# Optimization experiments

Measured on AMD Instinct MI355X. Metric: run time of the kernel, lower is better.

The kernel has to match this reference:

```python
import jax, jax.numpy as jnp
import numpy as np
from functools import partial

LEAK = 1.0 / 3.0   # scn default leakiness 0.333
EPS = 1e-4         # scn BatchNormalization default eps


def linkey(c, S):
    return (c[..., 0] * S + c[..., 1]) * S + c[..., 2]


def sub_offsets(K):
    r = K // 2
    g = np.stack(np.meshgrid(*([np.arange(-r, r + 1)] * 3), indexing='ij'), -1).reshape(-1, 3)
    return jnp.asarray(g, jnp.int32)


def down_offsets(s):
    g = np.stack(np.meshgrid(*([np.arange(s)] * 3), indexing='ij'), -1).reshape(-1, 3)
    return jnp.asarray(g, jnp.int32)


@partial(jax.checkpoint, static_argnums=(4, 5))
def sparse_conv(out_coords, in_coords, in_feats, W, S_in, stride, offsets):
    """Rulebook gather-GEMM-scatter via sorted-key binary search.
    out_coords [M,3], in_coords [N,3] sorted by linearized key, in_feats [N,Cin],
    W [K3,Cin,Cout]. Submanifold: stride=1, centered offsets, out_coords==in_coords.
    Strided scn.Convolution: offsets 0..stride-1, out sites = unique(in//stride)."""
    in_keys = linkey(in_coords, S_in)  # sorted [N]
    Nin = in_keys.shape[0]

    def body(acc, kw):
        off, Wk = kw
        child = out_coords * stride + off                       # [M,3]
        valid = jnp.all((child >= 0) & (child < S_in), axis=-1)
        nkey = linkey(child, S_in)
        idx = jnp.searchsorted(in_keys, nkey)
        idxc = jnp.clip(idx, 0, Nin - 1)
        found = valid & (in_keys[idxc] == nkey)
        g = jnp.where(found[:, None], in_feats[idxc], 0.0)      # gather, zero for inactive
        return acc + g @ Wk, None

    acc0 = jnp.zeros((out_coords.shape[0], W.shape[-1]), in_feats.dtype)
    acc, _ = jax.lax.scan(body, acc0, (offsets, W))
    return acc


def bn_lrelu(x, g, b):
    m = x.mean(0)
    v = x.var(0)
    y = (x - m) * (g / jnp.sqrt(v + EPS)) + b
    return jnp.where(y > 0, y, LEAK * y)


def lrelu(x):
    return jnp.where(x > 0, x, LEAK * x)


def forward_core(floats, c0, c1, c2, c3, c4):
    (feats0, W_init, Wd1, gd1, bd1, W11a, g11, b11, W11b,
     W12a, g12, b12, W12b, Wd2, gd2, bd2,
     W21a, g21, b21, W21b, W22a, g22, b22, W22b,
     Wd3, gd3, bd3, Wd4, gd4, bd4, W2, b2, W3, b3) = floats
    o3 = sub_offsets(3)
    x = sparse_conv(c0, c0, feats0, W_init, 512, 1, sub_offsets(7))                 # [N0,64] @512
    x = bn_lrelu(sparse_conv(c1, c0, x, Wd1, 512, 2, down_offsets(2)), gd1, bd1)    # [N1,64] @256
    res = x
    h = bn_lrelu(sparse_conv(c1, c1, x, W11a, 256, 1, o3), g11, b11)
    x = lrelu(sparse_conv(c1, c1, h, W11b, 256, 1, o3) + res)
    res = x
    h = bn_lrelu(sparse_conv(c1, c1, x, W12a, 256, 1, o3), g12, b12)
    x = lrelu(sparse_conv(c1, c1, h, W12b, 256, 1, o3) + res)
    x = bn_lrelu(sparse_conv(c2, c1, x, Wd2, 256, 2, down_offsets(2)), gd2, bd2)    # [N2,128] @128
    res = x
    h = bn_lrelu(sparse_conv(c2, c2, x, W21a, 128, 1, o3), g21, b21)
    x = lrelu(sparse_conv(c2, c2, h, W21b, 128, 1, o3) + res)
    res = x
    h = bn_lrelu(sparse_conv(c2, c2, x, W22a, 128, 1, o3), g22, b22)
    x = lrelu(sparse_conv(c2, c2, h, W22b, 128, 1, o3) + res)
    x = bn_lrelu(sparse_conv(c3, c2, x, Wd3, 128, 4, down_offsets(4)), gd3, bd3)    # [N3,64] @32
    x = bn_lrelu(sparse_conv(c4, c3, x, Wd4, 32, 4, down_offsets(4)), gd4, bd4)     # [N4,2]  @8
    # SparseToDense -> dense [2,8,8,8], then torch .view(-1, 2*8*8*8) (channel-major)
    k4 = linkey(c4, 8)
    dense = jnp.zeros((8 * 8 * 8, 2), x.dtype).at[k4].set(x)    # [512,2]
    flat = dense.T.reshape(1, -1)                               # [1,1024]
    v = jax.nn.elu(flat @ W2 + b2)
    return jax.nn.sigmoid(v @ W3 + b3)                          # [1,1]


def _decode(k, S):
    a = k // (S * S)
    r = k % (S * S)
    return np.stack([a, r // S, r % S], -1).astype(np.int32)


def setup_inputs() -> dict:
    rng = np.random.default_rng(0)
    N0 = 50000
    k0 = np.unique(rng.integers(0, 512 ** 3, size=N0 + 20000))[:N0]
    c0 = _decode(k0, 512)
    c1 = _decode(np.unique((c0[:, 0].astype(np.int64) // 2 * 256 + c0[:, 1] // 2) * 256 + c0[:, 2] // 2), 256)
    c2 = _decode(np.unique((c1[:, 0].astype(np.int64) // 2 * 128 + c1[:, 1] // 2) * 128 + c1[:, 2] // 2), 128)
    c3 = _decode(np.unique((c2[:, 0].astype(np.int64) // 4 * 32 + c2[:, 1] // 4) * 32 + c2[:, 2] // 4), 32)
    c4 = _decode(np.unique((c3[:, 0].astype(np.int64) // 4 * 8 + c3[:, 1] // 4) * 8 + c3[:, 2] // 4), 8)
    key = jax.random.key(0)
    ks = jax.random.split(key, 20)

    def w(i, shape, fan):
        return jax.random.normal(ks[i], shape, jnp.float32) / np.float32(np.sqrt(fan))

    return dict(
        feats0=jax.random.normal(ks[0], (N0, 1), jnp.float32),
        W_init=w(1, (343, 1, 64), 343.0),
        Wd1=w(2, (8, 64, 64), 8 * 64), gd1=jnp.ones(64), bd1=jnp.zeros(64),
        W11a=w(3, (27, 64, 64), 27 * 64), g11=jnp.ones(64), b11=jnp.zeros(64),
        W11b=w(4, (27, 64, 64), 27 * 64),
        W12a=w(5, (27, 64, 64), 27 * 64), g12=jnp.ones(64), b12=jnp.zeros(64),
        W12b=w(6, (27, 64, 64), 27 * 64),
        Wd2=w(7, (8, 64, 128), 8 * 64), gd2=jnp.ones(128), bd2=jnp.zeros(128),
        W21a=w(8, (27, 128, 128), 27 * 128), g21=jnp.ones(128), b21=jnp.zeros(128),
        W21b=w(9, (27, 128, 128), 27 * 128),
        W22a=w(10, (27, 128, 128), 27 * 128), g22=jnp.ones(128), b22=jnp.zeros(128),
        W22b=w(11, (27, 128, 128), 27 * 128),
        Wd3=w(12, (64, 128, 64), 64 * 128), gd3=jnp.ones(64), bd3=jnp.zeros(64),
        Wd4=w(13, (64, 64, 2), 64 * 64), gd4=jnp.ones(2), bd4=jnp.zeros(2),
        W2=w(14, (1024, 2), 1024.0), b2=jnp.zeros(2),
        W3=w(15, (2, 1), 2.0), b3=jnp.zeros(1),
        coords0=jnp.asarray(c0), coords1=jnp.asarray(c1), coords2=jnp.asarray(c2),
        coords3=jnp.asarray(c3), coords4=jnp.asarray(c4),
    )


def reference(feats0, W_init, Wd1, gd1, bd1, W11a, g11, b11, W11b, W12a, g12, b12, W12b,
              Wd2, gd2, bd2, W21a, g21, b21, W21b, W22a, g22, b22, W22b,
              Wd3, gd3, bd3, Wd4, gd4, bd4, W2, b2, W3, b3,
              coords0, coords1, coords2, coords3, coords4):
    floats = (feats0, W_init, Wd1, gd1, bd1, W11a, g11, b11, W11b, W12a, g12, b12, W12b,
              Wd2, gd2, bd2, W21a, g21, b21, W21b, W22a, g22, b22, W22b,
              Wd3, gd3, bd3, Wd4, gd4, bd4, W2, b2, W3, b3)
    return forward_core(floats, coords0, coords1, coords2, coords3, coords4)
```

## Files before the change

kernel.cpp:

```cpp
#include <hip/hip_runtime.h>

#define LEAKF (1.0f/3.0f)
#define BN_EPS 1e-4f

__device__ __forceinline__ unsigned hmix(int key) {
    unsigned h = (unsigned)key * 2654435761u;
    h ^= h >> 15;
    return h;
}

__device__ __forceinline__ int hlookup(const int* __restrict__ hk,
                                       const int* __restrict__ hv,
                                       int mask, int key) {
    unsigned h = hmix(key) & (unsigned)mask;
    while (true) {
        int k = hk[h];
        if (k == key) return hv[h];
        if (k == -1) return -1;
        h = (h + 1) & (unsigned)mask;
    }
}

__device__ __forceinline__ float bnl(float v, float s, float h) {
    v = v * s + h;
    return v > 0.f ? v : v * LEAKF;
}

__global__ __launch_bounds__(256) void build_hash_bm_all(
    int B0, int B1, int B2,
    int N0, const int* __restrict__ c0, int* __restrict__ hk0, int* __restrict__ hv0,
    int m0, unsigned* __restrict__ bm0,
    int N1, const int* __restrict__ c1, int* __restrict__ hk1, int* __restrict__ hv1,
    int m1, unsigned* __restrict__ bm1,
    int N2, const int* __restrict__ c2, int* __restrict__ hk2, int* __restrict__ hv2,
    int m2, unsigned* __restrict__ bm2,
    int N3, const int* __restrict__ c3, int* __restrict__ hk3, int* __restrict__ hv3,
    int m3) {
    const int* coords; int* hk; int* hv; unsigned* bm; int mask, S, N, i;
    int b = blockIdx.x;
    if (b < B0)           { coords = c0; hk = hk0; hv = hv0; bm = bm0; mask = m0; S = 512; N = N0; i = b * 256 + threadIdx.x; }
    else if (b < B0 + B1) { coords = c1; hk = hk1; hv = hv1; bm = bm1; mask = m1; S = 256; N = N1; i = (b - B0) * 256 + threadIdx.x; }
    else if (b < B0 + B1 + B2) { coords = c2; hk = hk2; hv = hv2; bm = bm2; mask = m2; S = 128; N = N2; i = (b - B0 - B1) * 256 + threadIdx.x; }
    else                  { coords = c3; hk = hk3; hv = hv3; bm = nullptr; mask = m3; S = 32; N = N3; i = (b - B0 - B1 - B2) * 256 + threadIdx.x; }
    if (i >= N) return;
    int key = (coords[3 * i] * S + coords[3 * i + 1]) * S + coords[3 * i + 2];
    if (bm) atomicOr(&bm[key >> 5], 1u << (key & 31));
    unsigned h = hmix(key) & (unsigned)mask;
    while (true) {
        int old = atomicCAS(&hk[h], -1, key);
        if (old == -1 || old == key) { hv[h] = i; break; }
        h = (h + 1) & (unsigned)mask;
    }
}

__global__ __launch_bounds__(256) void rb_sub_bm(
    int B1,
    int N1, const int* __restrict__ c1, const unsigned* __restrict__ bm1,
    const int* __restrict__ hk1, const int* __restrict__ hv1, int m1,
    int2* __restrict__ rb1, int* __restrict__ cnt1, int cap1,
    int N2, const int* __restrict__ c2, const unsigned* __restrict__ bm2,
    const int* __restrict__ hk2, const int* __restrict__ hv2, int m2,
    int2* __restrict__ rb2, int* __restrict__ cnt2, int cap2) {
    __shared__ int lcnt[27];
    __shared__ int lbase[27];
    int tid = threadIdx.x;
    if (tid < 27) lcnt[tid] = 0;
    __syncthreads();
    const int* coords; const unsigned* bm; const int* hk; const int* hv;
    int mask, S, N, t; int2* pairs; int* counts; int cap;
    if (blockIdx.x < B1) {
        coords = c1; bm = bm1; hk = hk1; hv = hv1; mask = m1; S = 256; N = N1;
        pairs = rb1; counts = cnt1; cap = cap1; t = blockIdx.x * 256 + tid;
    } else {
        coords = c2; bm = bm2; hk = hk2; hv = hv2; mask = m2; S = 128; N = N2;
        pairs = rb2; counts = cnt2; cap = cap2; t = (blockIdx.x - B1) * 256 + tid;
    }
    unsigned bits = 0;
    int m = 0, kmin = 0, z = 0, dx = 0, dy = 0;
    int rk[3], ix[3];
    if (t < N * 9) {
        m = t / 9;
        int od = t - m * 9;
        dx = od / 3 - 1;
        dy = od - (od / 3) * 3 - 1;
        int x = coords[3 * m] + dx;
        int y = coords[3 * m + 1] + dy;
        z = coords[3 * m + 2];
        if ((unsigned)x < (unsigned)S && (unsigned)y < (unsigned)S) {
            int zmin = z - 1 < 0 ? 0 : z - 1;
            int zmax = z + 1 > S - 1 ? S - 1 : z + 1;
            kmin = (x * S + y) * S + zmin;
            int wi = kmin >> 5, sh = kmin & 31, nb = zmax - zmin + 1;
            unsigned long long w =
                ((unsigned long long)bm[wi + 1] << 32) | (unsigned long long)bm[wi];
            bits = (unsigned)((w >> sh) & ((1u << nb) - 1u));
            if (dx == 0 && dy == 0) bits &= ~(1u << (z - zmin));
            unsigned tmp = bits;
            int nf = 0;
            while (tmp) {
                int bb = __ffs(tmp) - 1;
                tmp &= tmp - 1;
                ix[nf] = hlookup(hk, hv, mask, kmin + bb);
                int dz = (kmin & (S - 1)) + bb - z;
                int k = (dx + 1) * 9 + (dy + 1) * 3 + (dz + 1);
                rk[nf] = atomicAdd(&lcnt[k], 1);
                nf++;
            }
        }
    }
    __syncthreads();
    if (tid < 27 && lcnt[tid] > 0) lbase[tid] = atomicAdd(&counts[tid], lcnt[tid]);
    __syncthreads();
    {
        unsigned tmp = bits;
        int j = 0;
        while (tmp) {
            int bb = __ffs(tmp) - 1;
            tmp &= tmp - 1;
            int dz = (kmin & (S - 1)) + bb - z;
            int k = (dx + 1) * 9 + (dy + 1) * 3 + (dz + 1);
            int p = lbase[k] + rk[j];
            if (p < cap) pairs[(size_t)k * cap + p] = make_int2(m, ix[j]);
            j++;
        }
    }
}

__global__ __launch_bounds__(256) void rb_down_all(
    int B1, int B2,
    int N0, const int* __restrict__ c0, const int* __restrict__ hk1,
    const int* __restrict__ hv1, int m1, int2* __restrict__ rbD1,
    int* __restrict__ cntD1, int capD1,
    int N1, const int* __restrict__ c1, const int* __restrict__ hk2,
    const int* __restrict__ hv2, int m2, int2* __restrict__ rbD2,
    int* __restrict__ cntD2, int capD2,
    int N2, const int* __restrict__ c2, const int* __restrict__ hk3,
    const int* __restrict__ hv3, int m3, int2* __restrict__ rbD3,
    int* __restrict__ cntD3, int capD3) {
    __shared__ int lcnt[64];
    __shared__ int lbase[64];
    int tid = threadIdx.x;
    const int* cin; const int* hk; const int* hv;
    int mask, Sout, s, Nin, i; int2* pairs; int* counts; int cap;
    int b = blockIdx.x;
    if (b < B1) {
        cin = c0; hk = hk1; hv = hv1; mask = m1; Sout = 256; s = 2; Nin = N0;
        pairs = rbD1; counts = cntD1; cap = capD1; i = b * 256 + tid;
    } else if (b < B1 + B2) {
        cin = c1; hk = hk2; hv = hv2; mask = m2; Sout = 128; s = 2; Nin = N1;
        pairs = rbD2; counts = cntD2; cap = capD2; i = (b - B1) * 256 + tid;
    } else {
        cin = c2; hk = hk3; hv = hv3; mask = m3; Sout = 32; s = 4; Nin = N2;
        pairs = rbD3; counts = cntD3; cap = capD3; i = (b - B1 - B2) * 256 + tid;
    }
    int K3 = s * s * s;
    if (tid < K3) lcnt[tid] = 0;
    __syncthreads();
    int k = -1, m = -1, rank = 0;
    if (i < Nin) {
        int x = cin[3 * i], y = cin[3 * i + 1], z = cin[3 * i + 2];
        k = ((x % s) * s + (y % s)) * s + (z % s);
        int key = ((x / s) * Sout + (y / s)) * Sout + (z / s);
        m = hlookup(hk, hv, mask, key);
        rank = atomicAdd(&lcnt[k], 1);
    }
    __syncthreads();
    if (tid < K3 && lcnt[tid] > 0) lbase[tid] = atomicAdd(&counts[tid], lcnt[tid]);
    __syncthreads();
    if (i < Nin) {
        int p = lbase[k] + rank;
        if (p < cap) pairs[(size_t)k * cap + p] = make_int2(m, i);
    }
}

__global__ __launch_bounds__(256) void init_probe(
    int total, const int* __restrict__ c0, const unsigned* __restrict__ bm,
    const int* __restrict__ hk, const int* __restrict__ hv, int mask,
    int2* __restrict__ pairs, int* __restrict__ pcount, int cap) {
    __shared__ int lcnt, lbase;
    int tid = threadIdx.x;
    if (tid == 0) lcnt = 0;
    __syncthreads();
    int t = blockIdx.x * 256 + tid;
    unsigned bits = 0;
    int m = -1, kmin = 0, z = 0, dx = 0, dy = 0, rank = 0;
    if (t < total) {
        m = t / 49;
        int od = t - m * 49;
        dx = od / 7 - 3;
        dy = od - (od / 7) * 7 - 3;
        int x = c0[3 * m] + dx;
        int y = c0[3 * m + 1] + dy;
        z = c0[3 * m + 2];
        if ((unsigned)x < 512u && (unsigned)y < 512u) {
            int zmin = z - 3 < 0 ? 0 : z - 3;
            int zmax = z + 3 > 511 ? 511 : z + 3;
            kmin = (x * 512 + y) * 512 + zmin;
            int wi = kmin >> 5, sh = kmin & 31, nb = zmax - zmin + 1;
            unsigned long long w =
                ((unsigned long long)bm[wi + 1] << 32) | (unsigned long long)bm[wi];
            bits = (unsigned)((w >> sh) & ((1u << nb) - 1u));
            if (dx == 0 && dy == 0) bits &= ~(1u << (z - zmin));
            if (bits) rank = atomicAdd(&lcnt, __popc(bits));
        }
    }
    __syncthreads();
    if (tid == 0 && lcnt > 0) lbase = atomicAdd(pcount, lcnt);
    __syncthreads();
    while (bits) {
        int b = __ffs(bits) - 1;
        bits &= bits - 1;
        int nkey = kmin + b;
        int idx = hlookup(hk, hv, mask, nkey);
        int dz = (kmin & 511) + b - z;
        int k = (dx + 3) * 49 + (dy + 3) * 7 + (dz + 3);
        int p = lbase + rank++;
        if (p < cap) pairs[p] = make_int2(m, idx | (k << 17));
    }
}

__global__ __launch_bounds__(256) void init_center(
    int N0, const float* __restrict__ f0, const float* __restrict__ W,
    float* __restrict__ out) {
    int t = blockIdx.x * 256 + threadIdx.x;
    if (t >= N0 * 64) return;
    int m = t >> 6, co = t & 63;
    out[t] = f0[m] * W[171 * 64 + co];
}

__global__ __launch_bounds__(256) void init_apply(
    const int2* __restrict__ pairs, const int* __restrict__ pcount, int cap,
    const float* __restrict__ f0, const float* __restrict__ W,
    float* __restrict__ out) {
    int P = min(*pcount, cap);
    int t = blockIdx.x * 256 + threadIdx.x;
    if (t >= P * 64) return;
    int p = t >> 6, co = t & 63;
    int2 pr = pairs[p];
    int idx = pr.y & 0x1FFFF, k = pr.y >> 17;
    atomicAdd(&out[(size_t)pr.x * 64 + co], f0[idx] * W[k * 64 + co]);
}

template <int C, int TS, bool BNF>
__global__ __launch_bounds__(256) void center_gemm(
    int N, const float* __restrict__ inF, const float* __restrict__ Wc,
    float* __restrict__ out, const float* __restrict__ scp,
    const float* __restrict__ shp) {
    constexpr int C4 = C / 4;
    constexpr int SP = TS / 8;
    __shared__ float sW[C * 64];
    __shared__ float4 sRow[TS * C4];
    int tid = threadIdx.x;
    int t0 = blockIdx.x * TS;
    int co0 = blockIdx.y << 6;
    for (int e = tid; e < C * 16; e += 256) {
        int ci = e >> 4, c4 = e & 15;
        ((float4*)sW)[e] = *(const float4*)(Wc + (size_t)ci * C + co0 + c4 * 4);
    }
    for (int e = tid; e < TS * C4; e += 256) {
        int p = e / C4, c4 = e - p * C4;
        float4 v = make_float4(0.f, 0.f, 0.f, 0.f);
        if (t0 + p < N) {
            v = ((const float4*)inF)[(size_t)(t0 + p) * C4 + c4];
            if (BNF) {
                float4 s4 = ((const float4*)scp)[c4];
                float4 h4 = ((const float4*)shp)[c4];
                v.x = bnl(v.x, s4.x, h4.x);
                v.y = bnl(v.y, s4.y, h4.y);
                v.z = bnl(v.z, s4.z, h4.z);
                v.w = bnl(v.w, s4.w, h4.w);
            }
        }
        sRow[e] = v;
    }
    __syncthreads();
    int co = tid & 31, sg = tid >> 5;
    float accA[SP], accB[SP];
#pragma unroll
    for (int j = 0; j < SP; j++) { accA[j] = 0.f; accB[j] = 0.f; }
    for (int c4 = 0; c4 < C4; c4++) {
        float a0 = sW[(c4 * 4 + 0) * 64 + co];
        float a1 = sW[(c4 * 4 + 1) * 64 + co];
        float a2 = sW[(c4 * 4 + 2) * 64 + co];
        float a3 = sW[(c4 * 4 + 3) * 64 + co];
        float b0 = sW[(c4 * 4 + 0) * 64 + co + 32];
        float b1 = sW[(c4 * 4 + 1) * 64 + co + 32];
        float b2 = sW[(c4 * 4 + 2) * 64 + co + 32];
        float b3 = sW[(c4 * 4 + 3) * 64 + co + 32];
#pragma unroll
        for (int j = 0; j < SP; j++) {
            float4 r = sRow[(sg * SP + j) * C4 + c4];
            accA[j] += r.x * a0 + r.y * a1 + r.z * a2 + r.w * a3;
            accB[j] += r.x * b0 + r.y * b1 + r.z * b2 + r.w * b3;
        }
    }
#pragma unroll
    for (int j = 0; j < SP; j++) {
        int p = sg * SP + j;
        if (t0 + p < N) {
            out[(size_t)(t0 + p) * C + co0 + co] = accA[j];
            out[(size_t)(t0 + p) * C + co0 + co + 32] = accB[j];
        }
    }
}

template <int CIN, int P, bool BNF>
__global__ __launch_bounds__(256) void pair_gemm(
    const float* __restrict__ inF, const float* __restrict__ W, float* __restrict__ out,
    const int2* __restrict__ pairs, const int* __restrict__ counts,
    int cap, int chunksPerK, int COUT,
    const float* __restrict__ scp, const float* __restrict__ shp) {
    constexpr int C4 = CIN / 4;
    constexpr int SP = P / 8;
    __shared__ float sW[CIN * 64];
    __shared__ float4 sRow[P * C4];
    __shared__ int sM[P];
    __shared__ int sIdx[P];
    int k = blockIdx.x / chunksPerK;
    int chunk = blockIdx.x - k * chunksPerK;
    int cnt = min(counts[k], cap);
    int base = chunk * P;
    if (base >= cnt) return;
    int Pact = min(P, cnt - base);
    int tid = threadIdx.x;
    if (tid < P) {
        if (tid < Pact) {
            int2 pr = pairs[(size_t)k * cap + base + tid];
            sM[tid] = pr.x;
            sIdx[tid] = pr.y;
        } else {
            sM[tid] = -1;
            sIdx[tid] = 0;
        }
    }
    __syncthreads();
    int co0 = blockIdx.y << 6;
    const float* gW = W + (size_t)k * CIN * COUT + co0;
    for (int e = tid; e < CIN * 16; e += 256) {
        int ci = e >> 4, c4 = e & 15;
        ((float4*)sW)[e] = *(const float4*)(gW + (size_t)ci * COUT + c4 * 4);
    }
    for (int e = tid; e < P * C4; e += 256) {
        int p = e / C4, c4 = e - p * C4;
        float4 v = make_float4(0.f, 0.f, 0.f, 0.f);
        if (p < Pact) {
            v = ((const float4*)inF)[(size_t)sIdx[p] * C4 + c4];
            if (BNF) {
                float4 s4 = ((const float4*)scp)[c4];
                float4 h4 = ((const float4*)shp)[c4];
                v.x = bnl(v.x, s4.x, h4.x);
                v.y = bnl(v.y, s4.y, h4.y);
                v.z = bnl(v.z, s4.z, h4.z);
                v.w = bnl(v.w, s4.w, h4.w);
            }
        }
        sRow[e] = v;
    }
    __syncthreads();
    int co = tid & 31, sg = tid >> 5;
    float accA[SP], accB[SP];
#pragma unroll
    for (int j = 0; j < SP; j++) { accA[j] = 0.f; accB[j] = 0.f; }
    for (int c4 = 0; c4 < C4; c4++) {
        float a0 = sW[(c4 * 4 + 0) * 64 + co];
        float a1 = sW[(c4 * 4 + 1) * 64 + co];
        float a2 = sW[(c4 * 4 + 2) * 64 + co];
        float a3 = sW[(c4 * 4 + 3) * 64 + co];
        float b0 = sW[(c4 * 4 + 0) * 64 + co + 32];
        float b1 = sW[(c4 * 4 + 1) * 64 + co + 32];
        float b2 = sW[(c4 * 4 + 2) * 64 + co + 32];
        float b3 = sW[(c4 * 4 + 3) * 64 + co + 32];
#pragma unroll
        for (int j = 0; j < SP; j++) {
            float4 r = sRow[(sg * SP + j) * C4 + c4];
            accA[j] += r.x * a0 + r.y * a1 + r.z * a2 + r.w * a3;
            accB[j] += r.x * b0 + r.y * b1 + r.z * b2 + r.w * b3;
        }
    }
#pragma unroll
    for (int j = 0; j < SP; j++) {
        int p = sg * SP + j;
        if (p < Pact) {
            atomicAdd(&out[(size_t)sM[p] * COUT + co0 + co], accA[j]);
            atomicAdd(&out[(size_t)sM[p] * COUT + co0 + co + 32], accB[j]);
        }
    }
}

__global__ __launch_bounds__(64) void convd4_kernel(
    int M, const int* __restrict__ oc, const float* __restrict__ x3,
    const float* __restrict__ W, float* __restrict__ out4,
    const int* __restrict__ hk, const int* __restrict__ hv, int mask,
    const float* __restrict__ scp, const float* __restrict__ shp) {
    __shared__ int sIdx[64];
    __shared__ int sK[64];
    __shared__ int sCount;
    int m = blockIdx.x, tid = threadIdx.x;
    int cx = oc[3 * m], cy = oc[3 * m + 1], cz = oc[3 * m + 2];
    if (tid == 0) sCount = 0;
    __syncthreads();
    {
        int k = tid;
        int a = k >> 4, b = (k >> 2) & 3, c = k & 3;
        int x = cx * 4 + a, y = cy * 4 + b, z = cz * 4 + c;
        int key = (x * 32 + y) * 32 + z;
        int idx = hlookup(hk, hv, mask, key);
        if (idx >= 0) { int p = atomicAdd(&sCount, 1); sIdx[p] = idx; sK[p] = k; }
    }
    __syncthreads();
    int cnt = sCount;
    float s = scp[tid], h = shp[tid];
    float a0 = 0.f, a1 = 0.f;
    for (int j = 0; j < cnt; j++) {
        int idx = sIdx[j], k = sK[j];
        float f = bnl(x3[(size_t)idx * 64 + tid], s, h);
        const float* wk = W + ((size_t)k * 64 + tid) * 2;
        a0 += f * wk[0];
        a1 += f * wk[1];
    }
    for (int o = 32; o > 0; o >>= 1) {
        a0 += __shfl_down(a0, o);
        a1 += __shfl_down(a1, o);
    }
    if (tid == 0) { out4[2 * m] = a0; out4[2 * m + 1] = a1; }
}

__global__ __launch_bounds__(256) void bn_reduce_fin(
    const float4* __restrict__ X4, int total4, int B4, int C, int Cmask, float invN,
    const float* __restrict__ g, const float* __restrict__ b,
    float* __restrict__ sums, int* __restrict__ done,
    float* __restrict__ sc, float* __restrict__ sh) {
    __shared__ float sS[128];
    __shared__ float sQ[128];
    __shared__ int isLast;
    int tid = threadIdx.x;
    if (tid < C) { sS[tid] = 0.f; sQ[tid] = 0.f; }
    __syncthreads();
    int base4 = blockIdx.x * B4;
    int end4 = min(base4 + B4, total4);
    float s0 = 0.f, s1 = 0.f, s2 = 0.f, s3 = 0.f;
    float q0 = 0.f, q1 = 0.f, q2 = 0.f, q3 = 0.f;
    for (int e4 = base4 + tid; e4 < end4; e4 += 256) {
        float4 v = X4[e4];
        s0 += v.x; q0 += v.x * v.x;
        s1 += v.y; q1 += v.y * v.y;
        s2 += v.z; q2 += v.z * v.z;
        s3 += v.w; q3 += v.w * v.w;
    }
    int c0 = (4 * (base4 + tid)) & Cmask;
    atomicAdd(&sS[c0], s0);               atomicAdd(&sQ[c0], q0);
    atomicAdd(&sS[(c0 + 1) & Cmask], s1); atomicAdd(&sQ[(c0 + 1) & Cmask], q1);
    atomicAdd(&sS[(c0 + 2) & Cmask], s2); atomicAdd(&sQ[(c0 + 2) & Cmask], q2);
    atomicAdd(&sS[(c0 + 3) & Cmask], s3); atomicAdd(&sQ[(c0 + 3) & Cmask], q3);
    __syncthreads();
    if (tid < C) {
        atomicAdd(&sums[tid], sS[tid]);
        atomicAdd(&sums[128 + tid], sQ[tid]);
    }
    __syncthreads();
    if (tid == 0) {
        __threadfence();
        int t = atomicAdd(done, 1);
        isLast = (t == (int)gridDim.x - 1);
    }
    __syncthreads();
    if (isLast) {
        if (tid < C) {
            float v1 = atomicAdd(&sums[tid], 0.0f);
            float v2 = atomicAdd(&sums[128 + tid], 0.0f);
            float mean = v1 * invN;
            float var = v2 * invN - mean * mean;
            float s = g[tid] / sqrtf(var + BN_EPS);
            sc[tid] = s;
            sh[tid] = b[tid] - mean * s;
            sums[tid] = 0.f;
            sums[128 + tid] = 0.f;
        }
        if (tid == 0) *done = 0;
    }
}

__global__ __launch_bounds__(256) void add_lrelu(const float4* __restrict__ A,
                                                 const float4* __restrict__ R,
                                                 float4* __restrict__ Y, int total4) {
    int e = blockIdx.x * 256 + threadIdx.x;
    if (e >= total4) return;
    float4 a = A[e], r = R[e], v;
    v.x = a.x + r.x; v.y = a.y + r.y; v.z = a.z + r.z; v.w = a.w + r.w;
    v.x = v.x > 0.f ? v.x : v.x * LEAKF;
    v.y = v.y > 0.f ? v.y : v.y * LEAKF;
    v.z = v.z > 0.f ? v.z : v.z * LEAKF;
    v.w = v.w > 0.f ? v.w : v.w * LEAKF;
    Y[e] = v;
}

__global__ __launch_bounds__(256) void add_lrelu_bn(const float4* __restrict__ A,
                                                    const float4* __restrict__ X,
                                                    float4* __restrict__ Y, int total4,
                                                    int C4mask,
                                                    const float* __restrict__ scp,
                                                    const float* __restrict__ shp) {
    int e = blockIdx.x * 256 + threadIdx.x;
    if (e >= total4) return;
    int c4 = e & C4mask;
    float4 s4 = ((const float4*)scp)[c4];
    float4 h4 = ((const float4*)shp)[c4];
    float4 a = A[e], x = X[e], v;
    v.x = a.x + bnl(x.x, s4.x, h4.x);
    v.y = a.y + bnl(x.y, s4.y, h4.y);
    v.z = a.z + bnl(x.z, s4.z, h4.z);
    v.w = a.w + bnl(x.w, s4.w, h4.w);
    v.x = v.x > 0.f ? v.x : v.x * LEAKF;
    v.y = v.y > 0.f ? v.y : v.y * LEAKF;
    v.z = v.z > 0.f ? v.z : v.z * LEAKF;
    v.w = v.w > 0.f ? v.w : v.w * LEAKF;
    Y[e] = v;
}

__global__ __launch_bounds__(256) void bn_scatter(int M, const int* __restrict__ c4,
                                                  const float* __restrict__ x4,
                                                  const float* __restrict__ sc,
                                                  const float* __restrict__ sh,
                                                  float* __restrict__ dense) {
    int i = blockIdx.x * 256 + threadIdx.x;
    if (i >= 2 * M) return;
    int m = i >> 1, co = i & 1;
    float v = x4[i] * sc[co] + sh[co];
    v = v > 0.f ? v : v * LEAKF;
    int key = (c4[3 * m] * 8 + c4[3 * m + 1]) * 8 + c4[3 * m + 2];
    dense[key * 2 + co] = v;
}

__global__ __launch_bounds__(256) void head_kernel(const float* __restrict__ dense,
                                                   const float* __restrict__ W2,
                                                   const float* __restrict__ b2,
                                                   const float* __restrict__ W3,
                                                   const float* __restrict__ b3,
                                                   float* __restrict__ out) {
    __shared__ float r0[256];
    __shared__ float r1[256];
    int tid = threadIdx.x;
    float a0 = 0.f, a1 = 0.f;
    for (int j = tid; j < 1024; j += 256) {
        int co = j >> 9, k = j & 511;
        float f = dense[k * 2 + co];
        a0 += f * W2[2 * j];
        a1 += f * W2[2 * j + 1];
    }
    r0[tid] = a0;
    r1[tid] = a1;
    __syncthreads();
    for (int s = 128; s > 0; s >>= 1) {
        if (tid < s) { r0[tid] += r0[tid + s]; r1[tid] += r1[tid + s]; }
        __syncthreads();
    }
    if (tid == 0) {
        float v0 = r0[0] + b2[0];
        float v1 = r1[0] + b2[1];
        v0 = v0 > 0.f ? v0 : expm1f(v0);
        v1 = v1 > 0.f ? v1 : expm1f(v1);
        float z = v0 * W3[0] + v1 * W3[1] + b3[0];
        out[0] = 1.f / (1.f + expf(-z));
    }
}

extern "C" void kernel_launch(void* const* d_in, const int* in_sizes, int n_in,
                              void* d_out, int out_size, void* d_ws, size_t ws_size,
                              hipStream_t stream) {
    const float* F0    = (const float*)d_in[0];
    const float* Winit = (const float*)d_in[1];
    const float* Wd1   = (const float*)d_in[2];
    const float* gd1   = (const float*)d_in[3];
    const float* bd1   = (const float*)d_in[4];
    const float* W11a  = (const float*)d_in[5];
    const float* g11   = (const float*)d_in[6];
    const float* b11   = (const float*)d_in[7];
    const float* W11b  = (const float*)d_in[8];
    const float* W12a  = (const float*)d_in[9];
    const float* g12   = (const float*)d_in[10];
    const float* b12   = (const float*)d_in[11];
    const float* W12b  = (const float*)d_in[12];
    const float* Wd2   = (const float*)d_in[13];
    const float* gd2   = (const float*)d_in[14];
    const float* bd2   = (const float*)d_in[15];
    const float* W21a  = (const float*)d_in[16];
    const float* g21   = (const float*)d_in[17];
    const float* b21   = (const float*)d_in[18];
    const float* W21b  = (const float*)d_in[19];
    const float* W22a  = (const float*)d_in[20];
    const float* g22   = (const float*)d_in[21];
    const float* b22   = (const float*)d_in[22];
    const float* W22b  = (const float*)d_in[23];
    const float* Wd3   = (const float*)d_in[24];
    const float* gd3   = (const float*)d_in[25];
    const float* bd3   = (const float*)d_in[26];
    const float* Wd4   = (const float*)d_in[27];
    const float* gd4   = (const float*)d_in[28];
    const float* bd4   = (const float*)d_in[29];
    const float* W2    = (const float*)d_in[30];
    const float* b2    = (const float*)d_in[31];
    const float* W3    = (const float*)d_in[32];
    const float* b3    = (const float*)d_in[33];
    const int* c0 = (const int*)d_in[34];
    const int* c1 = (const int*)d_in[35];
    const int* c2 = (const int*)d_in[36];
    const int* c3 = (const int*)d_in[37];
    const int* c4 = (const int*)d_in[38];
    int N0 = in_sizes[34] / 3, N1 = in_sizes[35] / 3, N2 = in_sizes[36] / 3;
    int N3 = in_sizes[37] / 3, N4 = in_sizes[38] / 3;

    char* base = (char*)d_ws;
    size_t off = 0;
    auto alloc = [&](size_t bytes) -> void* {
        void* p = base + off;
        off = (off + bytes + 255) & ~(size_t)255;
        return p;
    };
    const int CAP0 = 262144, CAP = 131072, CAP3 = 65536;
    size_t hs_off = off;
    int* hk0 = (int*)alloc((size_t)CAP0 * 4);
    int* hv0 = (int*)alloc((size_t)CAP0 * 4);
    int* hk1 = (int*)alloc((size_t)CAP * 4);
    int* hv1 = (int*)alloc((size_t)CAP * 4);
    int* hk2 = (int*)alloc((size_t)CAP * 4);
    int* hv2 = (int*)alloc((size_t)CAP * 4);
    int* hk3 = (int*)alloc((size_t)CAP3 * 4);
    int* hv3 = (int*)alloc((size_t)CAP3 * 4);
    size_t he_off = off;
    size_t zs_off = off;
    float* sums = (float*)alloc(256 * 4);
    float* scb = (float*)alloc(8 * 128 * 4);
    float* shb = (float*)alloc(8 * 128 * 4);
    float* dense = (float*)alloc(1024 * 4);
    float* x4 = (float*)alloc(1032 * 4);
    int* counts = (int*)alloc(136 * 4);
    unsigned* bm1 = (unsigned*)alloc((size_t)(524288 + 2) * 4);
    unsigned* bm2 = (unsigned*)alloc((size_t)(65536 + 2) * 4);
    size_t ze_off = off;
    int* cntS1 = counts, *cntS2 = counts + 27, *cntD1 = counts + 54, *cntD2 = counts + 62,
       * cntD3 = counts + 70;
    int* done = counts + 134;
    int* pcount = counts + 135;
    const int CAP_S1 = 1024, CAP_S2 = 4096, CAP_D1 = 8192, CAP_D2 = 8192, CAP_D3 = 1024;
    const int CAPP = 16384;
    int2* pairs0 = (int2*)alloc((size_t)CAPP * 8);
    int2* rbS1 = (int2*)alloc((size_t)27 * CAP_S1 * 8);
    int2* rbS2 = (int2*)alloc((size_t)27 * CAP_S2 * 8);
    int2* rbD1 = (int2*)alloc((size_t)8 * CAP_D1 * 8);
    int2* rbD2 = (int2*)alloc((size_t)8 * CAP_D2 * 8);
    int2* rbD3 = (int2*)alloc((size_t)64 * CAP_D3 * 8);
    size_t relems = (size_t)N0 * 64;
    if ((size_t)N2 * 128 > relems) relems = (size_t)N2 * 128;
    float* R1 = (float*)alloc(relems * 4);
    float* R2 = (float*)alloc(relems * 4);
    float* R3 = (float*)alloc(relems * 4);
    unsigned* bm0 = (unsigned*)R1;

    hipMemsetAsync(base + hs_off, 0xFF, he_off - hs_off, stream);
    hipMemsetAsync(base + zs_off, 0x00, ze_off - zs_off, stream);
    hipMemsetAsync(bm0, 0x00, (size_t)(1 << 24) + 64, stream);

    int Bh0 = (N0 + 255) / 256, Bh1 = (N1 + 255) / 256, Bh2 = (N2 + 255) / 256,
        Bh3 = (N3 + 255) / 256;
    build_hash_bm_all<<<Bh0 + Bh1 + Bh2 + Bh3, 256, 0, stream>>>(
        Bh0, Bh1, Bh2,
        N0, c0, hk0, hv0, CAP0 - 1, bm0,
        N1, c1, hk1, hv1, CAP - 1, bm1,
        N2, c2, hk2, hv2, CAP - 1, bm2,
        N3, c3, hk3, hv3, CAP3 - 1);
    int Bs1 = (N1 * 9 + 255) / 256, Bs2 = (N2 * 9 + 255) / 256;
    rb_sub_bm<<<Bs1 + Bs2, 256, 0, stream>>>(
        Bs1,
        N1, c1, bm1, hk1, hv1, CAP - 1, rbS1, cntS1, CAP_S1,
        N2, c2, bm2, hk2, hv2, CAP - 1, rbS2, cntS2, CAP_S2);
    rb_down_all<<<Bh0 + Bh1 + Bh2, 256, 0, stream>>>(
        Bh0, Bh1,
        N0, c0, hk1, hv1, CAP - 1, rbD1, cntD1, CAP_D1,
        N1, c1, hk2, hv2, CAP - 1, rbD2, cntD2, CAP_D2,
        N2, c2, hk3, hv3, CAP3 - 1, rbD3, cntD3, CAP_D3);

    auto bnstats = [&](const float* X, int N, int C, const float* g, const float* b,
                       int slot) {
        int total4 = (N * C + 3) >> 2;
        int B4 = 32 * C;
        int grid = (total4 + B4 - 1) / B4;
        bn_reduce_fin<<<grid, 256, 0, stream>>>((const float4*)X, total4, B4, C, C - 1,
                                                1.0f / (float)N, g, b, sums, done,
                                                scb + slot * 128, shb + slot * 128);
    };
    auto sub64 = [&](const float* X, const float* W, float* Y, int slot) {
        if (slot >= 0) {
            center_gemm<64, 64, true><<<dim3((N1 + 63) / 64, 1), 256, 0, stream>>>(
                N1, X, W + 13 * 64 * 64, Y, scb + slot * 128, shb + slot * 128);
            pair_gemm<64, 64, true><<<dim3(27 * (CAP_S1 / 64), 1), 256, 0, stream>>>(
                X, W, Y, rbS1, cntS1, CAP_S1, CAP_S1 / 64, 64,
                scb + slot * 128, shb + slot * 128);
        } else {
            center_gemm<64, 64, false><<<dim3((N1 + 63) / 64, 1), 256, 0, stream>>>(
                N1, X, W + 13 * 64 * 64, Y, nullptr, nullptr);
            pair_gemm<64, 64, false><<<dim3(27 * (CAP_S1 / 64), 1), 256, 0, stream>>>(
                X, W, Y, rbS1, cntS1, CAP_S1, CAP_S1 / 64, 64, nullptr, nullptr);
        }
    };
    auto sub128 = [&](const float* X, const float* W, float* Y, int slot) {
        const int CH2 = (CAP_S2 + 47) / 48;
        if (slot >= 0) {
            center_gemm<128, 48, true><<<dim3((N2 + 47) / 48, 2), 256, 0, stream>>>(
                N2, X, W + 13 * 128 * 128, Y, scb + slot * 128, shb + slot * 128);
            pair_gemm<128, 48, true><<<dim3(27 * CH2, 2), 256, 0, stream>>>(
                X, W, Y, rbS2, cntS2, CAP_S2, CH2, 128, scb + slot * 128, shb + slot * 128);
        } else {
            center_gemm<128, 48, false><<<dim3((N2 + 47) / 48, 2), 256, 0, stream>>>(
                N2, X, W + 13 * 128 * 128, Y, nullptr, nullptr);
            pair_gemm<128, 48, false><<<dim3(27 * CH2, 2), 256, 0, stream>>>(
                X, W, Y, rbS2, cntS2, CAP_S2, CH2, 128, nullptr, nullptr);
        }
    };

    int totProbe = N0 * 49;
    init_probe<<<(totProbe + 255) / 256, 256, 0, stream>>>(totProbe, c0, bm0,
                                                           hk0, hv0, CAP0 - 1,
                                                           pairs0, pcount, CAPP);
    init_center<<<(N0 * 64 + 255) / 256, 256, 0, stream>>>(N0, F0, Winit, R3);
    init_apply<<<(CAPP * 64) / 256, 256, 0, stream>>>(pairs0, pcount, CAPP, F0, Winit, R3);

    hipMemsetAsync(R1, 0, (size_t)N1 * 64 * 4, stream);
    pair_gemm<64, 64, false><<<dim3(8 * (CAP_D1 / 64), 1), 256, 0, stream>>>(
        R3, Wd1, R1, rbD1, cntD1, CAP_D1, CAP_D1 / 64, 64, nullptr, nullptr);
    bnstats(R1, N1, 64, gd1, bd1, 0);

    sub64(R1, W11a, R2, 0);
    bnstats(R2, N1, 64, g11, b11, 1);
    sub64(R2, W11b, R3, 1);
    add_lrelu_bn<<<(N1 * 16 + 255) / 256, 256, 0, stream>>>(
        (const float4*)R3, (const float4*)R1, (float4*)R2, N1 * 16, 15, scb, shb);
    sub64(R2, W12a, R3, -1);
    bnstats(R3, N1, 64, g12, b12, 2);
    sub64(R3, W12b, R1, 2);
    add_lrelu<<<(N1 * 16 + 255) / 256, 256, 0, stream>>>(
        (const float4*)R1, (const float4*)R2, (float4*)R2, N1 * 16);

    hipMemsetAsync(R1, 0, (size_t)N2 * 128 * 4, stream);
    pair_gemm<64, 64, false><<<dim3(8 * (CAP_D2 / 64), 2), 256, 0, stream>>>(
        R2, Wd2, R1, rbD2, cntD2, CAP_D2, CAP_D2 / 64, 128, nullptr, nullptr);
    bnstats(R1, N2, 128, gd2, bd2, 3);

    sub128(R1, W21a, R2, 3);
    bnstats(R2, N2, 128, g21, b21, 4);
    sub128(R2, W21b, R3, 4);
    add_lrelu_bn<<<(N2 * 32 + 255) / 256, 256, 0, stream>>>(
        (const float4*)R3, (const float4*)R1, (float4*)R2, N2 * 32, 31,
        scb + 3 * 128, shb + 3 * 128);
    sub128(R2, W22a, R3, -1);
    bnstats(R3, N2, 128, g22, b22, 5);
    sub128(R3, W22b, R1, 5);
    add_lrelu<<<(N2 * 32 + 255) / 256, 256, 0, stream>>>(
        (const float4*)R1, (const float4*)R2, (float4*)R3, N2 * 32);

    hipMemsetAsync(R1, 0, (size_t)N3 * 64 * 4, stream);
    {
        const int CH3 = (CAP_D3 + 47) / 48;
        pair_gemm<128, 48, false><<<dim3(64 * CH3, 1), 256, 0, stream>>>(
            R3, Wd3, R1, rbD3, cntD3, CAP_D3, CH3, 64, nullptr, nullptr);
    }
    bnstats(R1, N3, 64, gd3, bd3, 6);

    convd4_kernel<<<N4, 64, 0, stream>>>(N4, c4, R1, Wd4, x4, hk3, hv3, CAP3 - 1,
                                         scb + 6 * 128, shb + 6 * 128);
    bnstats(x4, N4, 2, gd4, bd4, 7);
    bn_scatter<<<(2 * N4 + 255) / 256, 256, 0, stream>>>(N4, c4, x4, scb + 7 * 128,
                                                         shb + 7 * 128, dense);

    head_kernel<<<1, 256, 0, stream>>>(dense, W2, b2, W3, b3, (float*)d_out);
}
```

Baseline: 1.123 ms.

## Fuse residual add+LReLU into downsample gathers, enlarge GEMM tiles, swizzle probe blocks

Removes the two standalone add_lrelu kernels by computing residual add plus leaky ReLU on the fly while gathering rows in the following strided pair_gemm (new MODE=2). Buffer roles are reshuffled to match. Pair and center GEMM tile sizes grow (64→128 rows for C=64, 48→80 for C=128), and init_probe blocks are remapped in interleaved chunks of eight. Fusing saves a full read-write pass but recomputes the add for each of the 8 or 64 offsets. The larger tiles use more shared memory and registers per block.

```diff
diff --git a/kernel.cpp b/kernel.cpp
--- a/kernel.cpp
+++ b/kernel.cpp
@@ -174,14 +174,16 @@
 }
 
 __global__ __launch_bounds__(256) void init_probe(
-    int total, const int* __restrict__ c0, const unsigned* __restrict__ bm,
+    int total, int chunk, const int* __restrict__ c0, const unsigned* __restrict__ bm,
     const int* __restrict__ hk, const int* __restrict__ hv, int mask,
     int2* __restrict__ pairs, int* __restrict__ pcount, int cap) {
     __shared__ int lcnt, lbase;
     int tid = threadIdx.x;
     if (tid == 0) lcnt = 0;
     __syncthreads();
-    int t = blockIdx.x * 256 + tid;
+    int b = blockIdx.x;
+    int nb = (b & 7) * chunk + (b >> 3);
+    int t = nb * 256 + tid;
     unsigned bits = 0;
     int m = -1, kmin = 0, z = 0, dx = 0, dy = 0, rank = 0;
     if (t < total) {
@@ -196,10 +198,10 @@
             int zmin = z - 3 < 0 ? 0 : z - 3;
             int zmax = z + 3 > 511 ? 511 : z + 3;
             kmin = (x * 512 + y) * 512 + zmin;
-            int wi = kmin >> 5, sh = kmin & 31, nb = zmax - zmin + 1;
+            int wi = kmin >> 5, sh = kmin & 31, nb2 = zmax - zmin + 1;
             unsigned long long w =
                 ((unsigned long long)bm[wi + 1] << 32) | (unsigned long long)bm[wi];
-            bits = (unsigned)((w >> sh) & ((1u << nb) - 1u));
+            bits = (unsigned)((w >> sh) & ((1u << nb2) - 1u));
             if (dx == 0 && dy == 0) bits &= ~(1u << (z - zmin));
             if (bits) rank = atomicAdd(&lcnt, __popc(bits));
         }
@@ -208,11 +210,11 @@
     if (tid == 0 && lcnt > 0) lbase = atomicAdd(pcount, lcnt);
     __syncthreads();
     while (bits) {
-        int b = __ffs(bits) - 1;
+        int b2 = __ffs(bits) - 1;
         bits &= bits - 1;
-        int nkey = kmin + b;
+        int nkey = kmin + b2;
         int idx = hlookup(hk, hv, mask, nkey);
-        int dz = (kmin & 511) + b - z;
+        int dz = (kmin & 511) + b2 - z;
         int k = (dx + 3) * 49 + (dy + 3) * 7 + (dz + 3);
         int p = lbase + rank++;
         if (p < cap) pairs[p] = make_int2(m, idx | (k << 17));
@@ -304,9 +306,10 @@
     }
 }
 
-template <int CIN, int P, bool BNF>
+template <int CIN, int P, int MODE>
 __global__ __launch_bounds__(256) void pair_gemm(
-    const float* __restrict__ inF, const float* __restrict__ W, float* __restrict__ out,
+    const float* __restrict__ inF, const float* __restrict__ inF2,
+    const float* __restrict__ W, float* __restrict__ out,
     const int2* __restrict__ pairs, const int* __restrict__ counts,
     int cap, int chunksPerK, int COUT,
     const float* __restrict__ scp, const float* __restrict__ shp) {
@@ -345,13 +348,20 @@
         float4 v = make_float4(0.f, 0.f, 0.f, 0.f);
         if (p < Pact) {
             v = ((const float4*)inF)[(size_t)sIdx[p] * C4 + c4];
-            if (BNF) {
+            if (MODE == 1) {
                 float4 s4 = ((const float4*)scp)[c4];
                 float4 h4 = ((const float4*)shp)[c4];
                 v.x = bnl(v.x, s4.x, h4.x);
                 v.y = bnl(v.y, s4.y, h4.y);
                 v.z = bnl(v.z, s4.z, h4.z);
                 v.w = bnl(v.w, s4.w, h4.w);
+            } else if (MODE == 2) {
+                float4 u = ((const float4*)inF2)[(size_t)sIdx[p] * C4 + c4];
+                v.x += u.x; v.y += u.y; v.z += u.z; v.w += u.w;
+                v.x = v.x > 0.f ? v.x : v.x * LEAKF;
+                v.y = v.y > 0.f ? v.y : v.y * LEAKF;
+                v.z = v.z > 0.f ? v.z : v.z * LEAKF;
+                v.w = v.w > 0.f ? v.w : v.w * LEAKF;
             }
         }
         sRow[e] = v;
@@ -478,20 +488,6 @@
         }
         if (tid == 0) *done = 0;
     }
-}
-
-__global__ __launch_bounds__(256) void add_lrelu(const float4* __restrict__ A,
-                                                 const float4* __restrict__ R,
-                                                 float4* __restrict__ Y, int total4) {
-    int e = blockIdx.x * 256 + threadIdx.x;
-    if (e >= total4) return;
-    float4 a = A[e], r = R[e], v;
-    v.x = a.x + r.x; v.y = a.y + r.y; v.z = a.z + r.z; v.w = a.w + r.w;
-    v.x = v.x > 0.f ? v.x : v.x * LEAKF;
-    v.y = v.y > 0.f ? v.y : v.y * LEAKF;
-    v.z = v.z > 0.f ? v.z : v.z * LEAKF;
-    v.w = v.w > 0.f ? v.w : v.w * LEAKF;
-    Y[e] = v;
 }
 
 __global__ __launch_bounds__(256) void add_lrelu_bn(const float4* __restrict__ A,
@@ -688,45 +684,48 @@
                                                 1.0f / (float)N, g, b, sums, done,
                                                 scb + slot * 128, shb + slot * 128);
     };
+    const int CH_S1 = CAP_S1 / 128;
+    const int CH_S2 = (CAP_S2 + 79) / 80;
     auto sub64 = [&](const float* X, const float* W, float* Y, int slot) {
         if (slot >= 0) {
-            center_gemm<64, 64, true><<<dim3((N1 + 63) / 64, 1), 256, 0, stream>>>(
+            center_gemm<64, 128, true><<<dim3((N1 + 127) / 128, 1), 256, 0, stream>>>(
                 N1, X, W + 13 * 64 * 64, Y, scb + slot * 128, shb + slot * 128);
-            pair_gemm<64, 64, true><<<dim3(27 * (CAP_S1 / 64), 1), 256, 0, stream>>>(
-                X, W, Y, rbS1, cntS1, CAP_S1, CAP_S1 / 64, 64,
+            pair_gemm<64, 128, 1><<<dim3(27 * CH_S1, 1), 256, 0, stream>>>(
+                X, nullptr, W, Y, rbS1, cntS1, CAP_S1, CH_S1, 64,
                 scb + slot * 128, shb + slot * 128);
         } else {
-            center_gemm<64, 64, false><<<dim3((N1 + 63) / 64, 1), 256, 0, stream>>>(
+            center_gemm<64, 128, false><<<dim3((N1 + 127) / 128, 1), 256, 0, stream>>>(
                 N1, X, W + 13 * 64 * 64, Y, nullptr, nullptr);
-            pair_gemm<64, 64, false><<<dim3(27 * (CAP_S1 / 64), 1), 256, 0, stream>>>(
-                X, W, Y, rbS1, cntS1, CAP_S1, CAP_S1 / 64, 64, nullptr, nullptr);
+            pair_gemm<64, 128, 0><<<dim3(27 * CH_S1, 1), 256, 0, stream>>>(
+                X, nullptr, W, Y, rbS1, cntS1, CAP_S1, CH_S1, 64, nullptr, nullptr);
         }
     };
     auto sub128 = [&](const float* X, const float* W, float* Y, int slot) {
-        const int CH2 = (CAP_S2 + 47) / 48;
         if (slot >= 0) {
-            center_gemm<128, 48, true><<<dim3((N2 + 47) / 48, 2), 256, 0, stream>>>(
+            center_gemm<128, 80, true><<<dim3((N2 + 79) / 80, 2), 256, 0, stream>>>(
                 N2, X, W + 13 * 128 * 128, Y, scb + slot * 128, shb + slot * 128);
-            pair_gemm<128, 48, true><<<dim3(27 * CH2, 2), 256, 0, stream>>>(
-                X, W, Y, rbS2, cntS2, CAP_S2, CH2, 128, scb + slot * 128, shb + slot * 128);
+            pair_gemm<128, 80, 1><<<dim3(27 * CH_S2, 2), 256, 0, stream>>>(
+                X, nullptr, W, Y, rbS2, cntS2, CAP_S2, CH_S2, 128,
+                scb + slot * 128, shb + slot * 128);
         } else {
-            center_gemm<128, 48, false><<<dim3((N2 + 47) / 48, 2), 256, 0, stream>>>(
+            center_gemm<128, 80, false><<<dim3((N2 + 79) / 80, 2), 256, 0, stream>>>(
                 N2, X, W + 13 * 128 * 128, Y, nullptr, nullptr);
-            pair_gemm<128, 48, false><<<dim3(27 * CH2, 2), 256, 0, stream>>>(
-                X, W, Y, rbS2, cntS2, CAP_S2, CH2, 128, nullptr, nullptr);
+            pair_gemm<128, 80, 0><<<dim3(27 * CH_S2, 2), 256, 0, stream>>>(
+                X, nullptr, W, Y, rbS2, cntS2, CAP_S2, CH_S2, 128, nullptr, nullptr);
         }
     };
 
     int totProbe = N0 * 49;
-    init_probe<<<(totProbe + 255) / 256, 256, 0, stream>>>(totProbe, c0, bm0,
-                                                           hk0, hv0, CAP0 - 1,
-                                                           pairs0, pcount, CAPP);
+    int Gp = (totProbe + 255) / 256;
+    int chunkP = (Gp + 7) / 8;
+    init_probe<<<8 * chunkP, 256, 0, stream>>>(totProbe, chunkP, c0, bm0,
+                                               hk0, hv0, CAP0 - 1, pairs0, pcount, CAPP);
     init_center<<<(N0 * 64 + 255) / 256, 256, 0, stream>>>(N0, F0, Winit, R3);
     init_apply<<<(CAPP * 64) / 256, 256, 0, stream>>>(pairs0, pcount, CAPP, F0, Winit, R3);
 
     hipMemsetAsync(R1, 0, (size_t)N1 * 64 * 4, stream);
-    pair_gemm<64, 64, false><<<dim3(8 * (CAP_D1 / 64), 1), 256, 0, stream>>>(
-        R3, Wd1, R1, rbD1, cntD1, CAP_D1, CAP_D1 / 64, 64, nullptr, nullptr);
+    pair_gemm<64, 128, 0><<<dim3(8 * (CAP_D1 / 128), 1), 256, 0, stream>>>(
+        R3, nullptr, Wd1, R1, rbD1, cntD1, CAP_D1, CAP_D1 / 128, 64, nullptr, nullptr);
     bnstats(R1, N1, 64, gd1, bd1, 0);
 
     sub64(R1, W11a, R2, 0);
@@ -737,35 +736,31 @@
     sub64(R2, W12a, R3, -1);
     bnstats(R3, N1, 64, g12, b12, 2);
     sub64(R3, W12b, R1, 2);
-    add_lrelu<<<(N1 * 16 + 255) / 256, 256, 0, stream>>>(
-        (const float4*)R1, (const float4*)R2, (float4*)R2, N1 * 16);
-
-    hipMemsetAsync(R1, 0, (size_t)N2 * 128 * 4, stream);
-    pair_gemm<64, 64, false><<<dim3(8 * (CAP_D2 / 64), 2), 256, 0, stream>>>(
-        R2, Wd2, R1, rbD2, cntD2, CAP_D2, CAP_D2 / 64, 128, nullptr, nullptr);
-    bnstats(R1, N2, 128, gd2, bd2, 3);
-
-    sub128(R1, W21a, R2, 3);
-    bnstats(R2, N2, 128, g21, b21, 4);
-    sub128(R2, W21b, R3, 4);
+
+    hipMemsetAsync(R3, 0, (size_t)N2 * 128 * 4, stream);
+    pair_gemm<64, 128, 2><<<dim3(8 * (CAP_D2 / 128), 2), 256, 0, stream>>>(
+        R1, R2, Wd2, R3, rbD2, cntD2, CAP_D2, CAP_D2 / 128, 128, nullptr, nullptr);
+    bnstats(R3, N2, 128, gd2, bd2, 3);
+
+    sub128(R3, W21a, R1, 3);
+    bnstats(R1, N2, 128, g21, b21, 4);
+    sub128(R1, W21b, R2, 4);
     add_lrelu_bn<<<(N2 * 32 + 255) / 256, 256, 0, stream>>>(
-        (const float4*)R3, (const float4*)R1, (float4*)R2, N2 * 32, 31,
+        (const float4*)R2, (const float4*)R3, (float4*)R1, N2 * 32, 31,
         scb + 3 * 128, shb + 3 * 128);
-    sub128(R2, W22a, R3, -1);
-    bnstats(R3, N2, 128, g22, b22, 5);
-    sub128(R3, W22b, R1, 5);
-    add_lrelu<<<(N2 * 32 + 255) / 256, 256, 0, stream>>>(
-        (const float4*)R1, (const float4*)R2, (float4*)R3, N2 * 32);
-
-    hipMemsetAsync(R1, 0, (size_t)N3 * 64 * 4, stream);
+    sub128(R1, W22a, R2, -1);
+    bnstats(R2, N2, 128, g22, b22, 5);
+    sub128(R2, W22b, R3, 5);
+
+    hipMemsetAsync(R2, 0, (size_t)N3 * 64 * 4, stream);
     {
-        const int CH3 = (CAP_D3 + 47) / 48;
-        pair_gemm<128, 48, false><<<dim3(64 * CH3, 1), 256, 0, stream>>>(
-            R3, Wd3, R1, rbD3, cntD3, CAP_D3, CH3, 64, nullptr, nullptr);
-    }
-    bnstats(R1, N3, 64, gd3, bd3, 6);
-
-    convd4_kernel<<<N4, 64, 0, stream>>>(N4, c4, R1, Wd4, x4, hk3, hv3, CAP3 - 1,
+        const int CH3 = (CAP_D3 + 79) / 80;
+        pair_gemm<128, 80, 2><<<dim3(64 * CH3, 1), 256, 0, stream>>>(
+            R3, R1, Wd3, R2, rbD3, cntD3, CAP_D3, CH3, 64, nullptr, nullptr);
+    }
+    bnstats(R2, N3, 64, gd3, bd3, 6);
+
+    convd4_kernel<<<N4, 64, 0, stream>>>(N4, c4, R2, Wd4, x4, hk3, hv3, CAP3 - 1,
                                          scb + 6 * 128, shb + 6 * 128);
     bnstats(x4, N4, 2, gd4, bd4, 7);
     bn_scatter<<<(2 * N4 + 255) / 256, 256, 0, stream>>>(N4, c4, x4, scb + 7 * 128,
```

Result: no change. 1.134 ms (+1.0%).
